# Optimization experiments

Measured on AMD Instinct MI355X. Metric: run time of the kernel, lower is better.

The kernel has to match this reference:

```python
import jax, jax.numpy as jnp
import numpy as np

INPUT_SIZE = 256
HIDDEN_SIZE = 256

def setup_inputs() -> dict:
    key = jax.random.key(0)
    ks = jax.random.split(key, 10)
    B = 65536
    scale_in = 1.0 / np.sqrt(INPUT_SIZE)
    scale_h = 1.0 / np.sqrt(HIDDEN_SIZE)
    inp = {
        "x": jax.random.normal(ks[0], (B, INPUT_SIZE), dtype=jnp.float32),
        "h_prev": jax.random.normal(ks[1], (B, HIDDEN_SIZE), dtype=jnp.float32),
        # nn.Linear weights are [out, in]; torch computes x @ W.T
        "W_z": jax.random.uniform(ks[2], (HIDDEN_SIZE, INPUT_SIZE), jnp.float32, -scale_in, scale_in),
        "U_z": jax.random.uniform(ks[3], (HIDDEN_SIZE, HIDDEN_SIZE), jnp.float32, -scale_h, scale_h),
        "b_z": jnp.zeros((HIDDEN_SIZE,), dtype=jnp.float32),
        "W_a": jax.random.uniform(ks[4], (HIDDEN_SIZE, INPUT_SIZE), jnp.float32, -scale_in, scale_in),
        "U_a": jax.random.uniform(ks[5], (HIDDEN_SIZE, HIDDEN_SIZE), jnp.float32, -scale_h, scale_h),
        "v_a": jax.random.normal(ks[6], (HIDDEN_SIZE,), dtype=jnp.float32),
        "W_h": jax.random.uniform(ks[7], (HIDDEN_SIZE, INPUT_SIZE), jnp.float32, -scale_in, scale_in),
        "U_h": jax.random.uniform(ks[8], (HIDDEN_SIZE, HIDDEN_SIZE), jnp.float32, -scale_h, scale_h),
        "b_h": jnp.zeros((HIDDEN_SIZE,), dtype=jnp.float32),
    }
    return inp

def reference(x, h_prev, W_z, U_z, b_z, W_a, U_a, v_a, W_h, U_h, b_h):
    # update gate
    z_t = jax.nn.sigmoid(x @ W_z.T + h_prev @ U_z.T + b_z)  # [B, H]
    # attention-based reset replacement
    attention_input = jnp.tanh(x @ W_a.T + h_prev @ U_a.T)   # [B, H]
    attention_weights = jax.nn.softmax(attention_input * v_a, axis=-1)
    attended_h = attention_weights * h_prev                   # [B, H]
    # candidate state
    h_tilde = jnp.tanh(x @ W_h.T + attended_h @ U_h.T + b_h)  # [B, H]
    # blend
    h_t = (1.0 - z_t) * h_prev + z_t * h_tilde
    return h_t
```

## Files before the change

### kernel.cpp

```cpp
#include <hip/hip_runtime.h>

typedef __attribute__((ext_vector_type(8))) short  short8v;
typedef __attribute__((ext_vector_type(4))) float  float4v;

#define BDIM 512

__device__ ushort g_w[3 * 8 * 2048 * 8];

__device__ __forceinline__ ushort f2bf(float f) {
  unsigned u = __float_as_uint(f);
  u += 0x7fffu + ((u >> 16) & 1u);
  return (ushort)(u >> 16);
}
__device__ __forceinline__ float bf2f(ushort s) {
  return __uint_as_float(((unsigned)s) << 16);
}

__global__ __launch_bounds__(256) void conv_w(
    const float* __restrict__ Wz, const float* __restrict__ Uz,
    const float* __restrict__ Wa, const float* __restrict__ Ua,
    const float* __restrict__ Wh, const float* __restrict__ Uh)
{
  int tid = blockIdx.x * 256 + threadIdx.x;
  int p  = tid >> 14;
  int rm = tid & 16383;
  int kb = rm >> 11;
  int n  = (rm >> 3) & 255;
  int c  = rm & 7;
  const float* W = (p == 0) ? Wz : (p == 1) ? Wa : Wh;
  const float* U = (p == 0) ? Uz : (p == 1) ? Ua : Uh;
  int k0 = kb * 64 + ((c ^ (n & 7)) << 3);
  const float* src = (k0 < 256) ? (W + n * 256 + k0) : (U + n * 256 + k0 - 256);
  uint pk[4];
#pragma unroll
  for (int jj = 0; jj < 4; ++jj) {
    float v0 = src[jj * 2], v1 = src[jj * 2 + 1];
    pk[jj] = (uint)f2bf(v0) | ((uint)f2bf(v1) << 16);
  }
  *reinterpret_cast<uint4*>(&g_w[(size_t)tid * 8]) = make_uint4(pk[0], pk[1], pk[2], pk[3]);
}

__global__ __launch_bounds__(BDIM)
void gru_fused(
    const float* __restrict__ x,  const float* __restrict__ hp,
    const float* __restrict__ bz, const float* __restrict__ va,
    const float* __restrict__ bh, float* __restrict__ out)
{
  __shared__ __align__(16) ushort sA[64 * 512];
  __shared__ __align__(16) ushort sB[2][256 * 64];
  __shared__ __align__(16) float  sRed[2][64 * 8];

  const int tid  = threadIdx.x;
  const int w    = tid >> 6;
  const int lane = tid & 63;
  const int g4   = lane >> 4;
  const int l15  = lane & 15;
  const int sxor = l15 & 7;
  const int rowBlk = blockIdx.x << 6;

  auto stageB = [&](int blkid, int buf) {
    const char* sb = (const char*)g_w + ((size_t)blkid << 15) + (w << 12) + (lane << 4);
    char* db = ((char*)&sB[buf][0]) + (w << 12);
#pragma unroll
    for (int i = 0; i < 4; ++i) {
      __builtin_amdgcn_global_load_lds(
          (const __attribute__((address_space(1))) void*)(sb + i * 1024),
          (__attribute__((address_space(3))) void*)(db + i * 1024),
          16, 0, 0);
    }
  };

  stageB(0, 0);

  {
    const float4* xq = reinterpret_cast<const float4*>(x)  + (size_t)rowBlk * 64;
    const float4* hq = reinterpret_cast<const float4*>(hp) + (size_t)rowBlk * 64;
#pragma unroll
    for (int i = 0; i < 16; ++i) {
      int q   = tid + i * BDIM;
      int row = q >> 7;
      int qc  = q & 127;
      float4 v = (qc < 64) ? xq[row * 64 + qc] : hq[row * 64 + qc - 64];
      int kE  = qc << 2;
      int swz = (kE >> 3) ^ (row & 7);
      ushort4 pk4;
      pk4.x = f2bf(v.x); pk4.y = f2bf(v.y); pk4.z = f2bf(v.z); pk4.w = f2bf(v.w);
      *reinterpret_cast<ushort4*>((char*)sA + (row << 10) + (swz << 4) + ((kE & 7) << 1)) = pk4;
    }
  }
  __syncthreads();

  float4v acc[4][2];
  uint    zp[4][2][2];
  uint    hvp[4][2][2];
  int cur = 0;

  for (int p = 0; p < 3; ++p) {
#pragma unroll
    for (int m = 0; m < 4; ++m)
#pragma unroll
      for (int r = 0; r < 2; ++r)
        acc[m][r] = (float4v){0.f, 0.f, 0.f, 0.f};

    for (int kb = 0; kb < 8; ++kb) {
      int blk = p * 8 + kb;
      if (blk < 23) {
        stageB(blk + 1, cur ^ 1);
        asm volatile("s_waitcnt vmcnt(4)" ::: "memory");
      } else {
        asm volatile("s_waitcnt vmcnt(0)" ::: "memory");
      }

#pragma unroll
      for (int s = 0; s < 2; ++s) {
        short8v afr[4], bfr[2];
#pragma unroll
        for (int m = 0; m < 4; ++m) {
          int row = m * 16 + l15;
          int swz = (kb * 8 + s * 4 + g4) ^ sxor;
          afr[m] = *reinterpret_cast<const short8v*>((const char*)sA + (row << 10) + (swz << 4));
        }
#pragma unroll
        for (int r = 0; r < 2; ++r) {
          int n   = (w << 5) + (r << 4) + l15;
          int swz = (s * 4 + g4) ^ sxor;
          bfr[r] = *reinterpret_cast<const short8v*>((const char*)&sB[cur][0] + (n << 7) + (swz << 4));
        }
#pragma unroll
        for (int m = 0; m < 4; ++m)
#pragma unroll
          for (int r = 0; r < 2; ++r)
            acc[m][r] = __builtin_amdgcn_mfma_f32_16x16x32_bf16(afr[m], bfr[r], acc[m][r], 0, 0, 0);
      }

      __builtin_amdgcn_s_barrier();
      cur ^= 1;
    }

    if (p == 0) {
#pragma unroll
      for (int r = 0; r < 2; ++r) {
        float b = bz[(w << 5) + (r << 4) + l15];
#pragma unroll
        for (int m = 0; m < 4; ++m)
#pragma unroll
          for (int jj = 0; jj < 2; ++jj) {
            float z0 = 1.f / (1.f + __expf(-(acc[m][r][2 * jj]     + b)));
            float z1 = 1.f / (1.f + __expf(-(acc[m][r][2 * jj + 1] + b)));
            zp[m][r][jj] = (uint)f2bf(z0) | ((uint)f2bf(z1) << 16);
          }
      }
    } else if (p == 1) {
      float vav[2];
      vav[0] = va[(w << 5) + l15];
      vav[1] = va[(w << 5) + 16 + l15];
#pragma unroll
      for (int m = 0; m < 4; ++m)
#pragma unroll
        for (int r = 0; r < 2; ++r)
#pragma unroll
          for (int j = 0; j < 4; ++j) {
            float s = acc[m][r][j];
            float t = 1.f - 2.f / (__expf(2.f * s) + 1.f);
            acc[m][r][j] = t * vav[r];
          }
      float mx[4][4];
#pragma unroll
      for (int m = 0; m < 4; ++m)
#pragma unroll
        for (int j = 0; j < 4; ++j) {
          float v = fmaxf(acc[m][0][j], acc[m][1][j]);
          v = fmaxf(v, __shfl_xor(v, 1));
          v = fmaxf(v, __shfl_xor(v, 2));
          v = fmaxf(v, __shfl_xor(v, 4));
          v = fmaxf(v, __shfl_xor(v, 8));
          mx[m][j] = v;
        }
      if (l15 == 0) {
#pragma unroll
        for (int m = 0; m < 4; ++m)
#pragma unroll
          for (int j = 0; j < 4; ++j)
            sRed[0][((m * 16 + g4 * 4 + j) << 3) + w] = mx[m][j];
      }
      __syncthreads();
      float rmax[4][4];
#pragma unroll
      for (int m = 0; m < 4; ++m)
#pragma unroll
        for (int j = 0; j < 4; ++j) {
          int row = m * 16 + g4 * 4 + j;
          const float4* pr = reinterpret_cast<const float4*>(&sRed[0][row << 3]);
          float4 a = pr[0], b = pr[1];
          rmax[m][j] = fmaxf(fmaxf(fmaxf(a.x, a.y), fmaxf(a.z, a.w)),
                             fmaxf(fmaxf(b.x, b.y), fmaxf(b.z, b.w)));
        }
#pragma unroll
      for (int m = 0; m < 4; ++m)
#pragma unroll
        for (int j = 0; j < 4; ++j) {
          float e0 = __expf(acc[m][0][j] - rmax[m][j]);
          float e1 = __expf(acc[m][1][j] - rmax[m][j]);
          acc[m][0][j] = e0; acc[m][1][j] = e1;
          float sm = e0 + e1;
          sm += __shfl_xor(sm, 1);
          sm += __shfl_xor(sm, 2);
          sm += __shfl_xor(sm, 4);
          sm += __shfl_xor(sm, 8);
          if (l15 == 0) sRed[1][((m * 16 + g4 * 4 + j) << 3) + w] = sm;
        }
#pragma unroll
      for (int m = 0; m < 4; ++m)
#pragma unroll
        for (int r = 0; r < 2; ++r)
#pragma unroll
          for (int jj = 0; jj < 2; ++jj) {
            int row0 = m * 16 + g4 * 4 + 2 * jj;
            int row1 = row0 + 1;
            int cs0  = (32 + (w << 2) + (r << 1) + (l15 >> 3)) ^ (row0 & 7);
            int cs1  = (32 + (w << 2) + (r << 1) + (l15 >> 3)) ^ (row1 & 7);
            uint h0 = sA[(row0 << 9) + (cs0 << 3) + sxor];
            uint h1 = sA[(row1 << 9) + (cs1 << 3) + sxor];
            hvp[m][r][jj] = h0 | (h1 << 16);
          }
      __syncthreads();
#pragma unroll
      for (int m = 0; m < 4; ++m)
#pragma unroll
        for (int j = 0; j < 4; ++j) {
          int row = m * 16 + g4 * 4 + j;
          const float4* pr = reinterpret_cast<const float4*>(&sRed[1][row << 3]);
          float4 a = pr[0], b = pr[1];
          float s = (a.x + a.y) + (a.z + a.w) + (b.x + b.y) + (b.z + b.w);
          float inv = 1.f / s;
#pragma unroll
          for (int r = 0; r < 2; ++r) {
            uint hw = hvp[m][r][j >> 1];
            float hval = bf2f((ushort)((j & 1) ? (hw >> 16) : (hw & 0xffffu)));
            float at = acc[m][r][j] * inv * hval;
            int cs = (32 + (w << 2) + (r << 1) + (l15 >> 3)) ^ (row & 7);
            sA[(row << 9) + (cs << 3) + sxor] = f2bf(at);
          }
        }
      __syncthreads();
    } else {
#pragma unroll
      for (int r = 0; r < 2; ++r) {
        float b = bh[(w << 5) + (r << 4) + l15];
#pragma unroll
        for (int m = 0; m < 4; ++m)
#pragma unroll
          for (int j = 0; j < 4; ++j) {
            float s  = acc[m][r][j] + b;
            float ht = 1.f - 2.f / (__expf(2.f * s) + 1.f);
            uint zw  = zp[m][r][j >> 1];
            float z  = bf2f((ushort)((j & 1) ? (zw >> 16) : (zw & 0xffffu)));
            uint hw  = hvp[m][r][j >> 1];
            float h0 = bf2f((ushort)((j & 1) ? (hw >> 16) : (hw & 0xffffu)));
            float res = (1.f - z) * h0 + z * ht;
            int row = m * 16 + g4 * 4 + j;
            out[(size_t)(rowBlk + row) * 256 + (w << 5) + (r << 4) + l15] = res;
          }
      }
    }
  }
}

extern "C" void kernel_launch(void* const* d_in, const int* in_sizes, int n_in,
                              void* d_out, int out_size, void* d_ws, size_t ws_size,
                              hipStream_t stream)
{
  const float* x  = (const float*)d_in[0];
  const float* hp = (const float*)d_in[1];
  const float* Wz = (const float*)d_in[2];
  const float* Uz = (const float*)d_in[3];
  const float* bz = (const float*)d_in[4];
  const float* Wa = (const float*)d_in[5];
  const float* Ua = (const float*)d_in[6];
  const float* va = (const float*)d_in[7];
  const float* Wh = (const float*)d_in[8];
  const float* Uh = (const float*)d_in[9];
  const float* bh = (const float*)d_in[10];
  float* out = (float*)d_out;

  conv_w<<<dim3(192), dim3(256), 0, stream>>>(Wz, Uz, Wa, Ua, Wh, Uh);
  gru_fused<<<dim3(1024), dim3(BDIM), 0, stream>>>(x, hp, bz, va, bh, out);
}
```

Before: 406.6 us.

## Load weight fragments directly from global into registers, dropping LDS staging

Reorders the pre-converted bf16 weight buffer into MFMA fragment order, so each lane can load its B fragments straight from global memory (L2-resident) into registers, double-buffered one k-step ahead. This removes the LDS B staging buffers, the global_load_lds copies, the vmcnt waits and the per-k-block barriers, and frees LDS that may allow higher occupancy. In exchange, every block re-reads the weights from global or L2 per wave with no sharing through LDS, and load latency is hidden by only one k-step of register prefetch.

```diff
diff --git a/kernel.cpp b/kernel.cpp
--- a/kernel.cpp
+++ b/kernel.cpp
@@ -5,7 +5,7 @@
 
 #define BDIM 512
 
-__device__ ushort g_w[3 * 8 * 2048 * 8];
+__device__ ushort g_w[3 * 8 * 16 * 2 * 64 * 8];
 
 __device__ __forceinline__ ushort f2bf(float f) {
   unsigned u = __float_as_uint(f);
@@ -22,15 +22,16 @@
     const float* __restrict__ Wh, const float* __restrict__ Uh)
 {
   int tid = blockIdx.x * 256 + threadIdx.x;
-  int p  = tid >> 14;
-  int rm = tid & 16383;
-  int kb = rm >> 11;
-  int n  = (rm >> 3) & 255;
-  int c  = rm & 7;
+  int p   = tid >> 14;
+  int kb  = (tid >> 11) & 7;
+  int c16 = (tid >> 7) & 15;
+  int s   = (tid >> 6) & 1;
+  int l   = tid & 63;
   const float* W = (p == 0) ? Wz : (p == 1) ? Wa : Wh;
   const float* U = (p == 0) ? Uz : (p == 1) ? Ua : Uh;
-  int k0 = kb * 64 + ((c ^ (n & 7)) << 3);
-  const float* src = (k0 < 256) ? (W + n * 256 + k0) : (U + n * 256 + k0 - 256);
+  int col = c16 * 16 + (l & 15);
+  int k0  = kb * 64 + s * 32 + ((l >> 4) << 3);
+  const float* src = (k0 < 256) ? (W + col * 256 + k0) : (U + col * 256 + (k0 - 256));
   uint pk[4];
 #pragma unroll
   for (int jj = 0; jj < 4; ++jj) {
@@ -47,7 +48,6 @@
     const float* __restrict__ bh, float* __restrict__ out)
 {
   __shared__ __align__(16) ushort sA[64 * 512];
-  __shared__ __align__(16) ushort sB[2][256 * 64];
   __shared__ __align__(16) float  sRed[2][64 * 8];
 
   const int tid  = threadIdx.x;
@@ -58,19 +58,15 @@
   const int sxor = l15 & 7;
   const int rowBlk = blockIdx.x << 6;
 
-  auto stageB = [&](int blkid, int buf) {
-    const char* sb = (const char*)g_w + ((size_t)blkid << 15) + (w << 12) + (lane << 4);
-    char* db = ((char*)&sB[buf][0]) + (w << 12);
-#pragma unroll
-    for (int i = 0; i < 4; ++i) {
-      __builtin_amdgcn_global_load_lds(
-          (const __attribute__((address_space(1))) void*)(sb + i * 1024),
-          (__attribute__((address_space(3))) void*)(db + i * 1024),
-          16, 0, 0);
-    }
+  const ushort* wbase = g_w + (size_t)(w * 2048) + (size_t)lane * 8;
+  short8v bB[2][2];
+  auto loadBs = [&](int t, short8v* b) {
+    const ushort* pb = wbase + ((size_t)(t >> 1) << 14) + (size_t)((t & 1) << 9);
+    b[0] = *reinterpret_cast<const short8v*>(pb);
+    b[1] = *reinterpret_cast<const short8v*>(pb + 1024);
   };
 
-  stageB(0, 0);
+  loadBs(0, bB[0]);
 
   {
     const float4* xq = reinterpret_cast<const float4*>(x)  + (size_t)rowBlk * 64;
@@ -93,7 +89,6 @@
   float4v acc[4][2];
   uint    zp[4][2][2];
   uint    hvp[4][2][2];
-  int cur = 0;
 
   for (int p = 0; p < 3; ++p) {
 #pragma unroll
@@ -102,18 +97,13 @@
       for (int r = 0; r < 2; ++r)
         acc[m][r] = (float4v){0.f, 0.f, 0.f, 0.f};
 
+#pragma unroll
     for (int kb = 0; kb < 8; ++kb) {
-      int blk = p * 8 + kb;
-      if (blk < 23) {
-        stageB(blk + 1, cur ^ 1);
-        asm volatile("s_waitcnt vmcnt(4)" ::: "memory");
-      } else {
-        asm volatile("s_waitcnt vmcnt(0)" ::: "memory");
-      }
-
 #pragma unroll
       for (int s = 0; s < 2; ++s) {
-        short8v afr[4], bfr[2];
+        if ((kb * 2 + s < 15) || (p < 2))
+          loadBs(p * 16 + kb * 2 + s + 1, bB[s ^ 1]);
+        short8v afr[4];
 #pragma unroll
         for (int m = 0; m < 4; ++m) {
           int row = m * 16 + l15;
@@ -121,20 +111,11 @@
           afr[m] = *reinterpret_cast<const short8v*>((const char*)sA + (row << 10) + (swz << 4));
         }
 #pragma unroll
-        for (int r = 0; r < 2; ++r) {
-          int n   = (w << 5) + (r << 4) + l15;
-          int swz = (s * 4 + g4) ^ sxor;
-          bfr[r] = *reinterpret_cast<const short8v*>((const char*)&sB[cur][0] + (n << 7) + (swz << 4));
-        }
-#pragma unroll
         for (int m = 0; m < 4; ++m)
 #pragma unroll
           for (int r = 0; r < 2; ++r)
-            acc[m][r] = __builtin_amdgcn_mfma_f32_16x16x32_bf16(afr[m], bfr[r], acc[m][r], 0, 0, 0);
-      }
-
-      __builtin_amdgcn_s_barrier();
-      cur ^= 1;
+            acc[m][r] = __builtin_amdgcn_mfma_f32_16x16x32_bf16(afr[m], bB[s][r], acc[m][r], 0, 0, 0);
+      }
     }
 
     if (p == 0) {
```

After: 373.4 us. -8.2%, faster.
